# Kernel tuning notes

Hardware: AMD Instinct MI355X
Metric: run time of the kernel (lower is better)

## Reference

```python
import jax, jax.numpy as jnp
import numpy as np

B, S, D = 512, 8, 1024
L = 6        # n_layers
LOOPS = 4    # n_loops
EPS = 1e-5   # LayerNorm eps (torch default)


def setup_inputs() -> dict:
    key = jax.random.key(0)
    ks = jax.random.split(key, 8)
    s = 1.0 / np.sqrt(D)  # torch Linear default init bound
    x = jax.random.normal(ks[0], (B, S, D), jnp.float32)
    gamma = jnp.ones((L, D), jnp.float32)
    beta = jnp.zeros((L, D), jnp.float32)
    Wg = jax.random.uniform(ks[1], (L, D, D), jnp.float32, -s, s)
    bg = jax.random.uniform(ks[2], (L, D), jnp.float32, -s, s)
    Wt = jax.random.uniform(ks[3], (L, D, D), jnp.float32, -s, s)
    bt = jax.random.uniform(ks[4], (L, D), jnp.float32, -s, s)
    Wc = jax.random.uniform(ks[5], (D, 1), jnp.float32, -s, s)
    bc = jax.random.uniform(ks[6], (1,), jnp.float32, -s, s)
    return {"x": x, "gamma": gamma, "beta": beta, "Wg": Wg, "bg": bg,
            "Wt": Wt, "bt": bt, "Wc": Wc, "bc": bc}


def _block(x, gamma, beta, Wg, bg, Wt, bt):
    # LayerNorm over last dim
    mu = jnp.mean(x, axis=-1, keepdims=True)
    var = jnp.mean(jnp.square(x - mu), axis=-1, keepdims=True)
    xn = (x - mu) * jax.lax.rsqrt(var + EPS) * gamma + beta
    g = jax.nn.sigmoid(jnp.einsum('bsd,de->bse', xn, Wg) + bg)
    t = jnp.tanh(jnp.einsum('bsd,de->bse', xn, Wt) + bt)
    return x * (1.0 - g) + t * g


def reference(x, gamma, beta, Wg, bg, Wt, bt, Wc, bc):
    confs = []
    for _ in range(LOOPS):
        for i in range(L):
            x = _block(x, gamma[i], beta[i], Wg[i], bg[i], Wt[i], bt[i])
        # confidence = sigmoid(Linear(x.mean(dim=1)))  -> (B, 1)
        confs.append(jax.nn.sigmoid(x.mean(axis=1) @ Wc + bc))
    return x, jnp.stack(confs)  # ((B,S,D), (LOOPS,B,1))
```

## Files before the change

### kernel.cpp

```cpp
#include <hip/hip_runtime.h>
#include <hip/hip_bf16.h>
#include <math.h>

#define B_ 512
#define S_ 8
#define D_ 1024
#define L_ 6
#define LOOPS_ 4
#define R_ (B_*S_)
#define LD_ (L_*D_)
#define EPSV 1e-5f

#define BM 128
#define BN 128
#define BK 64
#define NT (D_/BK)
#define A_USH 8192
#define B_USH 16384

typedef __attribute__((ext_vector_type(4))) float f32x4;
typedef __attribute__((ext_vector_type(8))) _Float16 f16x8;

__device__ __forceinline__ float bf2f(unsigned short u){
  union { float f; unsigned int i; } v; v.i = ((unsigned int)u) << 16; return v.f;
}
__device__ __forceinline__ unsigned short f2h(float f){
  _Float16 h = (_Float16)f;
  union { _Float16 h; unsigned short u; } v; v.h = h; return v.u;
}
__device__ __forceinline__ float h2f(unsigned short u){
  union { unsigned short u; _Float16 h; } v; v.u = u; return (float)v.h;
}
__device__ __forceinline__ float loadf(const void* p, size_t i, int bf){
  return bf ? bf2f(((const unsigned short*)p)[i]) : ((const float*)p)[i];
}
__device__ __forceinline__ void gload16(const void* g, void* l){
  __builtin_amdgcn_global_load_lds((const __attribute__((address_space(1))) void*)g,
                                   (__attribute__((address_space(3))) void*)l, 16, 0, 0);
}

__global__ void k_detect(const unsigned int* __restrict__ gamma_raw, int* __restrict__ flag){
  if (threadIdx.x == 0 && blockIdx.x == 0)
    *flag = (gamma_raw[0] == 0x3F803F80u) ? 1 : 0;
}

__global__ void k_x2f(const void* __restrict__ x, float* __restrict__ xf,
                      const int* __restrict__ flag, int n4){
  int i = blockIdx.x * blockDim.x + threadIdx.x;
  if (i >= n4) return;
  if (*flag){
    ushort4 u = ((const ushort4*)x)[i];
    float4 f; f.x = bf2f(u.x); f.y = bf2f(u.y); f.z = bf2f(u.z); f.w = bf2f(u.w);
    ((float4*)xf)[i] = f;
  } else {
    ((float4*)xf)[i] = ((const float4*)x)[i];
  }
}

__global__ void k_small(const void* g, const void* b, const void* bgp, const void* btp,
                        const void* wcp, const void* bcp,
                        float* __restrict__ sm, const int* __restrict__ flag){
  int i = blockIdx.x * blockDim.x + threadIdx.x;
  int bf = *flag;
  if (i < LD_)               sm[i] = loadf(g,   i,          bf);
  else if (i < 2*LD_)        sm[i] = loadf(b,   i - LD_,    bf);
  else if (i < 3*LD_)        sm[i] = loadf(bgp, i - 2*LD_,  bf);
  else if (i < 4*LD_)        sm[i] = loadf(btp, i - 3*LD_,  bf);
  else if (i < 4*LD_ + D_)   sm[i] = loadf(wcp, i - 4*LD_,  bf);
  else if (i == 4*LD_ + D_)  sm[i] = loadf(bcp, 0,          bf);
}

__global__ void k_transpose(const void* __restrict__ Wg, const void* __restrict__ Wt,
                            ushort* __restrict__ WgT, ushort* __restrict__ WtT,
                            const float* __restrict__ sm, const int* __restrict__ flag){
  __shared__ ushort tile[32][33];
  int bf = *flag;
  int z = blockIdx.z;
  const void* src; ushort* dst; int lz;
  size_t base;
  if (z < L_) { src = Wg; dst = WgT + (size_t)z * D_ * D_;        base = (size_t)z * D_ * D_; lz = z; }
  else        { src = Wt; dst = WtT + (size_t)(z - L_) * D_ * D_; base = (size_t)(z - L_) * D_ * D_; lz = z - L_; }
  int d0 = blockIdx.y * 32, e0 = blockIdx.x * 32;
  int tx = threadIdx.x, ty = threadIdx.y;
  #pragma unroll
  for (int i = 0; i < 4; i++){
    int r = ty + i * 8;
    size_t idx = base + (size_t)(d0 + r) * D_ + e0 + tx;
    float v = bf ? bf2f(((const ushort*)src)[idx]) : ((const float*)src)[idx];
    float gv = sm[(size_t)lz * D_ + d0 + r];
    tile[r][tx] = f2h(gv * v);
  }
  __syncthreads();
  #pragma unroll
  for (int i = 0; i < 4; i++){
    int r = ty + i * 8;
    dst[(size_t)(e0 + r) * D_ + d0 + tx] = tile[tx][r];
  }
}

__global__ __launch_bounds__(256) void k_bias(const ushort* __restrict__ WgT, const ushort* __restrict__ WtT,
                      const float* __restrict__ sm, float* __restrict__ bias2){
  int idx = blockIdx.x * 256 + threadIdx.x;
  int mat = idx / LD_;
  int rem = idx - mat * LD_;
  int l = rem >> 10, e = rem & 1023;
  const ushort* WT = (mat ? WtT : WgT) + (size_t)l * D_ * D_ + (size_t)e * D_;
  const float* beta = sm + LD_ + (size_t)l * D_;
  float acc = sm[(size_t)(2 + mat) * LD_ + rem];
  for (int d = 0; d < D_; d++)
    acc += beta[d] * h2f(WT[d]);
  bias2[idx] = acc;
}

__device__ __forceinline__ void stage_Bh(const ushort* __restrict__ wsrc,
    ushort* __restrict__ dstbase, int nbase, int kb, int w, int lane)
{
  int rr = lane >> 3;
  int clog = (lane & 7) ^ rr;
  int coff = kb + clog * 8;
  int r0 = w * 16;
  gload16(wsrc + (size_t)(nbase + r0 + rr) * D_ + coff,     dstbase + r0 * 64);
  gload16(wsrc + (size_t)(nbase + r0 + 8 + rr) * D_ + coff, dstbase + (r0 + 8) * 64);
}

__global__ __launch_bounds__(512, 2) void k_gemm_gate(
    const float* __restrict__ xin, float* __restrict__ xout,
    const ushort* __restrict__ WgT, const ushort* __restrict__ WtT,
    const float* __restrict__ bgf, const float* __restrict__ btf)
{
  __shared__ __align__(16) ushort smem[2 * A_USH + 3 * B_USH];

  const int t = threadIdx.x;
  const int lane = t & 63, w = t >> 6;
  const int wrr = (w >> 2) * 64, wnn = (w & 3) * 32;
  const int l15 = lane & 15;

  int bid = blockIdx.x;
  int swz = (bid & 7) * 32 + (bid >> 3);
  int mbase = (swz >> 3) * BM;
  int nbase = (swz & 7) * BN;

  ushort* Abuf = smem;
  ushort* Bbuf = smem + 2 * A_USH;

  float mu = 0.f, rs = 0.f;
  {
    const float* xb = xin + (size_t)(mbase + w * 16) * D_;
    for (int j = 0; j < 16; j++){
      float s = 0.f, q = 0.f;
      #pragma unroll
      for (int p = 0; p < 4; p++){
        float4 v = *(const float4*)(xb + (size_t)j * D_ + p * 256 + lane * 4);
        s += v.x + v.y + v.z + v.w;
        q += v.x * v.x + v.y * v.y + v.z * v.z + v.w * v.w;
      }
      #pragma unroll
      for (int o = 32; o; o >>= 1){ s += __shfl_xor(s, o); q += __shfl_xor(q, o); }
      float m = s * (1.0f / D_);
      float r2 = rsqrtf(q * (1.0f / D_) - m * m + EPSV);
      if ((lane >> 2) == j){ mu = m; rs = r2; }
    }
  }

  const int ar = t >> 2, cq = t & 3;
  const float* xrow = xin + (size_t)(mbase + ar) * D_;

  f32x4 accg[4][2], acct[4][2];
  #pragma unroll
  for (int i = 0; i < 4; i++)
    #pragma unroll
    for (int j = 0; j < 2; j++){
      accg[i][j] = (f32x4){0.f, 0.f, 0.f, 0.f};
      acct[i][j] = (f32x4){0.f, 0.f, 0.f, 0.f};
    }

  float4 ra[4];
  f16x8 af0[4], bg0[2], bt0[2];
  f16x8 af1[4], bg1[2], bt1[2];

  #pragma unroll
  for (int i = 0; i < 2; i++)
    #pragma unroll
    for (int j = 0; j < 2; j++)
      ra[i * 2 + j] = *(const float4*)(xrow + (cq + i * 4) * 8 + j * 4);
  stage_Bh(WgT, Bbuf, nbase, 0, w, lane);
  stage_Bh(WtT, Bbuf + 8192, nbase, 0, w, lane);
  stage_Bh(WgT, Bbuf + B_USH, nbase, BK, w, lane);
  stage_Bh(WtT, Bbuf + B_USH + 8192, nbase, BK, w, lane);
  asm volatile("s_waitcnt vmcnt(8)" ::: "memory");
  #pragma unroll
  for (int i = 0; i < 2; i++){
    int c = cq + i * 4;
    float4 a0 = ra[i * 2], a1 = ra[i * 2 + 1];
    f16x8 hv;
    hv[0] = (_Float16)((a0.x - mu) * rs); hv[1] = (_Float16)((a0.y - mu) * rs);
    hv[2] = (_Float16)((a0.z - mu) * rs); hv[3] = (_Float16)((a0.w - mu) * rs);
    hv[4] = (_Float16)((a1.x - mu) * rs); hv[5] = (_Float16)((a1.y - mu) * rs);
    hv[6] = (_Float16)((a1.z - mu) * rs); hv[7] = (_Float16)((a1.w - mu) * rs);
    *(f16x8*)(Abuf + ar * 64 + ((c ^ (ar & 7)) << 3)) = hv;
  }
  asm volatile("s_waitcnt vmcnt(4)" ::: "memory");
  __builtin_amdgcn_s_barrier();
  {
    int cl = (lane >> 4);
    #pragma unroll
    for (int mf = 0; mf < 4; mf++){
      int r = wrr + mf * 16 + l15;
      af0[mf] = *(const f16x8*)(Abuf + r * 64 + ((cl ^ (r & 7)) << 3));
    }
    #pragma unroll
    for (int nf = 0; nf < 2; nf++){
      int r = wnn + nf * 16 + l15;
      int off = r * 64 + ((cl ^ (r & 7)) << 3);
      bg0[nf] = *(const f16x8*)(Bbuf + off);
      bt0[nf] = *(const f16x8*)(Bbuf + 8192 + off);
    }
  }

  for (int kt = 0; kt < NT; ++kt){
    ushort* Ab = Abuf + (kt & 1) * A_USH;
    ushort* An = Abuf + ((kt + 1) & 1) * A_USH;
    ushort* Bb = Bbuf + (kt % 3) * B_USH;
    ushort* Bn1 = Bbuf + ((kt + 1) % 3) * B_USH;
    ushort* Bn2 = Bbuf + ((kt + 2) % 3) * B_USH;

    {
      int cl = 4 + (lane >> 4);
      #pragma unroll
      for (int mf = 0; mf < 4; mf++){
        int r = wrr + mf * 16 + l15;
        af1[mf] = *(const f16x8*)(Ab + r * 64 + ((cl ^ (r & 7)) << 3));
      }
      #pragma unroll
      for (int nf = 0; nf < 2; nf++){
        int r = wnn + nf * 16 + l15;
        int off = r * 64 + ((cl ^ (r & 7)) << 3);
        bg1[nf] = *(const f16x8*)(Bb + off);
        bt1[nf] = *(const f16x8*)(Bb + 8192 + off);
      }
    }
    if (kt + 1 < NT){
      int kb = (kt + 1) * BK;
      #pragma unroll
      for (int i = 0; i < 2; i++)
        #pragma unroll
        for (int j = 0; j < 2; j++)
          ra[i * 2 + j] = *(const float4*)(xrow + kb + (cq + i * 4) * 8 + j * 4);
    }
    if (kt + 2 < NT) stage_Bh(WgT, Bn2, nbase, (kt + 2) * BK, w, lane);
    __builtin_amdgcn_s_setprio(1);
    #pragma unroll
    for (int mf = 0; mf < 4; mf++)
      #pragma unroll
      for (int nf = 0; nf < 2; nf++){
        accg[mf][nf] = __builtin_amdgcn_mfma_f32_16x16x32_f16(af0[mf], bg0[nf], accg[mf][nf], 0, 0, 0);
        acct[mf][nf] = __builtin_amdgcn_mfma_f32_16x16x32_f16(af0[mf], bt0[nf], acct[mf][nf], 0, 0, 0);
      }
    __builtin_amdgcn_s_setprio(0);

    if (kt + 2 < NT) stage_Bh(WtT, Bn2 + 8192, nbase, (kt + 2) * BK, w, lane);
    if (kt + 1 < NT){
      if (kt == NT - 2) asm volatile("s_waitcnt vmcnt(0)" ::: "memory");
      else              asm volatile("s_waitcnt vmcnt(4)" ::: "memory");
      #pragma unroll
      for (int i = 0; i < 2; i++){
        int c = cq + i * 4;
        float4 a0 = ra[i * 2], a1 = ra[i * 2 + 1];
        f16x8 hv;
        hv[0] = (_Float16)((a0.x - mu) * rs); hv[1] = (_Float16)((a0.y - mu) * rs);
        hv[2] = (_Float16)((a0.z - mu) * rs); hv[3] = (_Float16)((a0.w - mu) * rs);
        hv[4] = (_Float16)((a1.x - mu) * rs); hv[5] = (_Float16)((a1.y - mu) * rs);
        hv[6] = (_Float16)((a1.z - mu) * rs); hv[7] = (_Float16)((a1.w - mu) * rs);
        *(f16x8*)(An + ar * 64 + ((c ^ (ar & 7)) << 3)) = hv;
      }
    }
    __builtin_amdgcn_s_barrier();
    if (kt + 1 < NT){
      int cl = (lane >> 4);
      #pragma unroll
      for (int mf = 0; mf < 4; mf++){
        int r = wrr + mf * 16 + l15;
        af0[mf] = *(const f16x8*)(An + r * 64 + ((cl ^ (r & 7)) << 3));
      }
      #pragma unroll
      for (int nf = 0; nf < 2; nf++){
        int r = wnn + nf * 16 + l15;
        int off = r * 64 + ((cl ^ (r & 7)) << 3);
        bg0[nf] = *(const f16x8*)(Bn1 + off);
        bt0[nf] = *(const f16x8*)(Bn1 + 8192 + off);
      }
    }
    __builtin_amdgcn_s_setprio(1);
    #pragma unroll
    for (int mf = 0; mf < 4; mf++)
      #pragma unroll
      for (int nf = 0; nf < 2; nf++){
        accg[mf][nf] = __builtin_amdgcn_mfma_f32_16x16x32_f16(af1[mf], bg1[nf], accg[mf][nf], 0, 0, 0);
        acct[mf][nf] = __builtin_amdgcn_mfma_f32_16x16x32_f16(af1[mf], bt1[nf], acct[mf][nf], 0, 0, 0);
      }
    __builtin_amdgcn_s_setprio(0);
  }

  #pragma unroll
  for (int mf = 0; mf < 4; mf++){
    int row0 = mbase + wrr + mf * 16 + ((lane >> 4) * 4);
    #pragma unroll
    for (int nf = 0; nf < 2; nf++){
      int col = nbase + wnn + nf * 16 + l15;
      float bgv = bgf[col];
      float btv = btf[col];
      #pragma unroll
      for (int j = 0; j < 4; j++){
        float ug = accg[mf][nf][j] + bgv;
        float ut = acct[mf][nf][j] + btv;
        float g = 1.0f / (1.0f + expf(-ug));
        float tt = tanhf(ut);
        size_t idx = (size_t)(row0 + j) * D_ + col;
        float xo = xin[idx];
        xout[idx] = xo + g * (tt - xo);
      }
    }
  }
}

__global__ __launch_bounds__(256) void k_conf(const float* __restrict__ xf, const float* __restrict__ Wc,
                       const float* __restrict__ bc, float* __restrict__ out, int loop){
  int b = blockIdx.x;
  int t = threadIdx.x;
  const float* xb = xf + (size_t)b * S_ * D_;
  float acc = 0.f;
  for (int i = t; i < S_ * D_; i += 256){
    int d = i & (D_ - 1);
    acc += xb[i] * Wc[d];
  }
  #pragma unroll
  for (int o = 32; o; o >>= 1) acc += __shfl_xor(acc, o);
  __shared__ float wsum[4];
  int w = t >> 6, lane = t & 63;
  if (lane == 0) wsum[w] = acc;
  __syncthreads();
  if (t == 0){
    float s = wsum[0] + wsum[1] + wsum[2] + wsum[3];
    float z = s * (1.0f / S_) + bc[0];
    float c = 1.0f / (1.0f + expf(-z));
    out[(size_t)R_ * D_ + (size_t)loop * B_ + b] = c;
  }
}

__global__ void k_f2x(const float* __restrict__ xf, float* __restrict__ out, int n4){
  int i = blockIdx.x * blockDim.x + threadIdx.x;
  if (i >= n4) return;
  ((float4*)out)[i] = ((const float4*)xf)[i];
}

extern "C" void kernel_launch(void* const* d_in, const int* in_sizes, int n_in,
                              void* d_out, int out_size, void* d_ws, size_t ws_size,
                              hipStream_t stream){
  const void* x     = d_in[0];
  const void* gamma = d_in[1];
  const void* beta  = d_in[2];
  const void* Wg    = d_in[3];
  const void* bg    = d_in[4];
  const void* Wt    = d_in[5];
  const void* bt    = d_in[6];
  const void* Wc    = d_in[7];
  const void* bc    = d_in[8];
  float* out = (float*)d_out;

  char* ws = (char*)d_ws;
  float*  xfA = (float*)ws;
  float*  xfB = xfA + (size_t)R_ * D_;
  ushort* WgT = (ushort*)(xfB + (size_t)R_ * D_);
  ushort* WtT = WgT + (size_t)L_ * D_ * D_;
  float*  sm  = (float*)(WtT + (size_t)L_ * D_ * D_);
  float*  bias2 = sm + 4 * LD_ + D_ + 1;
  int*    flag  = (int*)(bias2 + 2 * LD_);

  k_detect<<<1, 64, 0, stream>>>((const unsigned int*)gamma, flag);
  k_small<<<(4 * LD_ + D_ + 1 + 255) / 256, 256, 0, stream>>>(gamma, beta, bg, bt, Wc, bc, sm, flag);
  k_x2f<<<4096, 256, 0, stream>>>(x, xfA, flag, R_ * D_ / 4);
  dim3 tb(32, 8); dim3 tg(D_ / 32, D_ / 32, 2 * L_);
  k_transpose<<<tg, tb, 0, stream>>>(Wg, Wt, WgT, WtT, sm, flag);
  k_bias<<<2 * LD_ / 256, 256, 0, stream>>>(WgT, WtT, sm, bias2);

  const float* smWc = sm + 4 * LD_;
  const float* smBc = sm + 4 * LD_ + D_;

  for (int loop = 0; loop < LOOPS_; ++loop){
    for (int l = 0; l < L_; ++l){
      int step = loop * L_ + l;
      const float* xin = (step & 1) ? xfB : xfA;
      float*       xo  = (step & 1) ? xfA : xfB;
      k_gemm_gate<<<256, 512, 0, stream>>>(xin, xo,
                                           WgT + (size_t)l * D_ * D_, WtT + (size_t)l * D_ * D_,
                                           bias2 + (size_t)l * D_, bias2 + (size_t)(L_ + l) * D_);
    }
    k_conf<<<B_, 256, 0, stream>>>(xfA, smWc, smBc, out, loop);
  }
  k_f2x<<<4096, 256, 0, stream>>>(xfA, out, R_ * D_ / 4);
}
```

Baseline: 1.060 ms.

## Fuse LayerNorm row statistics into GEMM epilogue and restructure k-loop pipeline

Each gated GEMM now writes per-row partial sums and sums of squares for its output column block. The next layer reads these eight partials instead of re-reading whole rows of x to compute LayerNorm statistics, and the initial conversion kernel produces the first set. The main loop is reorganised to load both k-substeps at once and stage Wg/Wt together, launch bounds change to one block per CU, and sigmoid/tanh use fast __expf forms. The bias precompute is also parallelised across a wavefront. The trade-off is extra shuffle and shared-memory reductions in the epilogue, and a different register and occupancy profile.

```diff
diff --git a/kernel.cpp b/kernel.cpp
--- a/kernel.cpp
+++ b/kernel.cpp
@@ -28,9 +28,6 @@
   _Float16 h = (_Float16)f;
   union { _Float16 h; unsigned short u; } v; v.h = h; return v.u;
 }
-__device__ __forceinline__ float h2f(unsigned short u){
-  union { unsigned short u; _Float16 h; } v; v.u = u; return (float)v.h;
-}
 __device__ __forceinline__ float loadf(const void* p, size_t i, int bf){
   return bf ? bf2f(((const unsigned short*)p)[i]) : ((const float*)p)[i];
 }
@@ -38,23 +35,47 @@
   __builtin_amdgcn_global_load_lds((const __attribute__((address_space(1))) void*)g,
                                    (__attribute__((address_space(3))) void*)l, 16, 0, 0);
 }
+__device__ __forceinline__ float fsigmoid(float u){
+  return 1.0f / (1.0f + __expf(-u));
+}
+__device__ __forceinline__ float ftanh(float u){
+  return 1.0f - 2.0f / (__expf(2.0f * u) + 1.0f);
+}
 
 __global__ void k_detect(const unsigned int* __restrict__ gamma_raw, int* __restrict__ flag){
   if (threadIdx.x == 0 && blockIdx.x == 0)
     *flag = (gamma_raw[0] == 0x3F803F80u) ? 1 : 0;
 }
 
-__global__ void k_x2f(const void* __restrict__ x, float* __restrict__ xf,
-                      const int* __restrict__ flag, int n4){
-  int i = blockIdx.x * blockDim.x + threadIdx.x;
-  if (i >= n4) return;
+__global__ __launch_bounds__(256) void k_x2f(const void* __restrict__ x, float* __restrict__ xf,
+                      const int* __restrict__ flag, float* __restrict__ st0){
+  int row = blockIdx.x, t = threadIdx.x;
+  size_t i4 = (size_t)row * 256 + t;
+  float4 v;
   if (*flag){
-    ushort4 u = ((const ushort4*)x)[i];
-    float4 f; f.x = bf2f(u.x); f.y = bf2f(u.y); f.z = bf2f(u.z); f.w = bf2f(u.w);
-    ((float4*)xf)[i] = f;
+    ushort4 u = ((const ushort4*)x)[i4];
+    v.x = bf2f(u.x); v.y = bf2f(u.y); v.z = bf2f(u.z); v.w = bf2f(u.w);
   } else {
-    ((float4*)xf)[i] = ((const float4*)x)[i];
-  }
+    v = ((const float4*)x)[i4];
+  }
+  ((float4*)xf)[i4] = v;
+  float s = v.x + v.y + v.z + v.w;
+  float q = v.x * v.x + v.y * v.y + v.z * v.z + v.w * v.w;
+  #pragma unroll
+  for (int o = 32; o; o >>= 1){ s += __shfl_xor(s, o); q += __shfl_xor(q, o); }
+  __shared__ float ss[4], qq[4];
+  int w = t >> 6, lane = t & 63;
+  if (lane == 0){ ss[w] = s; qq[w] = q; }
+  __syncthreads();
+  if (t == 0){
+    st0[(size_t)row * 2]     = ss[0] + ss[1] + ss[2] + ss[3];
+    st0[(size_t)row * 2 + 1] = qq[0] + qq[1] + qq[2] + qq[3];
+  }
+}
+
+__global__ void k_zstat(float* __restrict__ statsA){
+  int i = blockIdx.x * 256 + threadIdx.x;
+  statsA[2 * R_ + i] = 0.f;
 }
 
 __global__ void k_small(const void* g, const void* b, const void* bgp, const void* btp,
@@ -100,70 +121,74 @@
 
 __global__ __launch_bounds__(256) void k_bias(const ushort* __restrict__ WgT, const ushort* __restrict__ WtT,
                       const float* __restrict__ sm, float* __restrict__ bias2){
-  int idx = blockIdx.x * 256 + threadIdx.x;
+  int w = threadIdx.x >> 6, lane = threadIdx.x & 63;
+  int idx = blockIdx.x * 4 + w;
   int mat = idx / LD_;
   int rem = idx - mat * LD_;
   int l = rem >> 10, e = rem & 1023;
-  const ushort* WT = (mat ? WtT : WgT) + (size_t)l * D_ * D_ + (size_t)e * D_;
-  const float* beta = sm + LD_ + (size_t)l * D_;
-  float acc = sm[(size_t)(2 + mat) * LD_ + rem];
-  for (int d = 0; d < D_; d++)
-    acc += beta[d] * h2f(WT[d]);
-  bias2[idx] = acc;
-}
-
-__device__ __forceinline__ void stage_Bh(const ushort* __restrict__ wsrc,
-    ushort* __restrict__ dstbase, int nbase, int kb, int w, int lane)
+  const ushort* WT = (mat ? WtT : WgT) + (size_t)l * D_ * D_ + (size_t)e * D_ + lane * 16;
+  const float* beta = sm + LD_ + (size_t)l * D_ + lane * 16;
+  float acc = 0.f;
+  #pragma unroll
+  for (int i = 0; i < 2; i++){
+    f16x8 hv = *(const f16x8*)(WT + i * 8);
+    #pragma unroll
+    for (int j = 0; j < 8; j++) acc += beta[i * 8 + j] * (float)hv[j];
+  }
+  #pragma unroll
+  for (int o = 32; o; o >>= 1) acc += __shfl_xor(acc, o);
+  if (lane == 0) bias2[idx] = sm[(size_t)(2 + mat) * LD_ + rem] + acc;
+}
+
+__device__ __forceinline__ void stage_B(const ushort* __restrict__ wg, const ushort* __restrict__ wt,
+    ushort* __restrict__ bbase, int nbase, int kb, int w, int lane)
 {
-  int rr = lane >> 3;
-  int clog = (lane & 7) ^ rr;
-  int coff = kb + clog * 8;
+  int rr = lane >> 3, sl = lane & 7;
+  int coff = kb + ((sl ^ rr) << 3);
   int r0 = w * 16;
-  gload16(wsrc + (size_t)(nbase + r0 + rr) * D_ + coff,     dstbase + r0 * 64);
-  gload16(wsrc + (size_t)(nbase + r0 + 8 + rr) * D_ + coff, dstbase + (r0 + 8) * 64);
-}
-
-__global__ __launch_bounds__(512, 2) void k_gemm_gate(
+  gload16(wg + (size_t)(nbase + r0 + rr) * D_ + coff,     bbase + r0 * 64);
+  gload16(wg + (size_t)(nbase + r0 + 8 + rr) * D_ + coff, bbase + (r0 + 8) * 64);
+  gload16(wt + (size_t)(nbase + r0 + rr) * D_ + coff,     bbase + 8192 + r0 * 64);
+  gload16(wt + (size_t)(nbase + r0 + 8 + rr) * D_ + coff, bbase + 8192 + (r0 + 8) * 64);
+}
+
+__global__ __launch_bounds__(512, 1) void k_gemm_gate(
     const float* __restrict__ xin, float* __restrict__ xout,
     const ushort* __restrict__ WgT, const ushort* __restrict__ WtT,
-    const float* __restrict__ bgf, const float* __restrict__ btf)
+    const float* __restrict__ bgf, const float* __restrict__ btf,
+    const float* __restrict__ stin, float* __restrict__ stout)
 {
   __shared__ __align__(16) ushort smem[2 * A_USH + 3 * B_USH];
+  __shared__ __align__(8) float2 sred[4][128];
 
   const int t = threadIdx.x;
   const int lane = t & 63, w = t >> 6;
-  const int wrr = (w >> 2) * 64, wnn = (w & 3) * 32;
-  const int l15 = lane & 15;
+  const int wr = w >> 2, wn = w & 3;
+  const int l15 = lane & 15, q4 = lane >> 4;
 
   int bid = blockIdx.x;
   int swz = (bid & 7) * 32 + (bid >> 3);
   int mbase = (swz >> 3) * BM;
   int nbase = (swz & 7) * BN;
-
-  ushort* Abuf = smem;
+  int nb = swz & 7;
+
   ushort* Bbuf = smem + 2 * A_USH;
 
-  float mu = 0.f, rs = 0.f;
-  {
-    const float* xb = xin + (size_t)(mbase + w * 16) * D_;
-    for (int j = 0; j < 16; j++){
-      float s = 0.f, q = 0.f;
-      #pragma unroll
-      for (int p = 0; p < 4; p++){
-        float4 v = *(const float4*)(xb + (size_t)j * D_ + p * 256 + lane * 4);
-        s += v.x + v.y + v.z + v.w;
-        q += v.x * v.x + v.y * v.y + v.z * v.z + v.w * v.w;
-      }
-      #pragma unroll
-      for (int o = 32; o; o >>= 1){ s += __shfl_xor(s, o); q += __shfl_xor(q, o); }
-      float m = s * (1.0f / D_);
-      float r2 = rsqrtf(q * (1.0f / D_) - m * m + EPSV);
-      if ((lane >> 2) == j){ mu = m; rs = r2; }
-    }
-  }
-
-  const int ar = t >> 2, cq = t & 3;
-  const float* xrow = xin + (size_t)(mbase + ar) * D_;
+  const int rr8 = lane >> 3, sl = lane & 7;
+  const int ar1 = w * 16 + rr8, ar2 = ar1 + 8;
+  const int clog = sl ^ rr8;
+  float s1 = 0.f, q1 = 0.f, s2 = 0.f, q2 = 0.f;
+  #pragma unroll
+  for (int nb2 = 0; nb2 < 8; nb2++){
+    float2 v1 = *(const float2*)(stin + ((size_t)nb2 * R_ + mbase + ar1) * 2);
+    float2 v2 = *(const float2*)(stin + ((size_t)nb2 * R_ + mbase + ar2) * 2);
+    s1 += v1.x; q1 += v1.y; s2 += v2.x; q2 += v2.y;
+  }
+  float mu1 = s1 * (1.0f / D_), rs1 = rsqrtf(q1 * (1.0f / D_) - mu1 * mu1 + EPSV);
+  float mu2 = s2 * (1.0f / D_), rs2 = rsqrtf(q2 * (1.0f / D_) - mu2 * mu2 + EPSV);
+
+  const float* xr1 = xin + (size_t)(mbase + ar1) * D_ + clog * 8;
+  const float* xr2 = xin + (size_t)(mbase + ar2) * D_ + clog * 8;
 
   f32x4 accg[4][2], acct[4][2];
   #pragma unroll
@@ -174,152 +199,135 @@
       acct[i][j] = (f32x4){0.f, 0.f, 0.f, 0.f};
     }
 
-  float4 ra[4];
-  f16x8 af0[4], bg0[2], bt0[2];
-  f16x8 af1[4], bg1[2], bt1[2];
-
-  #pragma unroll
-  for (int i = 0; i < 2; i++)
-    #pragma unroll
-    for (int j = 0; j < 2; j++)
-      ra[i * 2 + j] = *(const float4*)(xrow + (cq + i * 4) * 8 + j * 4);
-  stage_Bh(WgT, Bbuf, nbase, 0, w, lane);
-  stage_Bh(WtT, Bbuf + 8192, nbase, 0, w, lane);
-  stage_Bh(WgT, Bbuf + B_USH, nbase, BK, w, lane);
-  stage_Bh(WtT, Bbuf + B_USH + 8192, nbase, BK, w, lane);
+  float4 ra0, ra1, ra2, ra3;
+
+  ra0 = *(const float4*)(xr1);     ra1 = *(const float4*)(xr1 + 4);
+  ra2 = *(const float4*)(xr2);     ra3 = *(const float4*)(xr2 + 4);
+  stage_B(WgT, WtT, Bbuf, nbase, 0, w, lane);
+  stage_B(WgT, WtT, Bbuf + B_USH, nbase, BK, w, lane);
   asm volatile("s_waitcnt vmcnt(8)" ::: "memory");
-  #pragma unroll
-  for (int i = 0; i < 2; i++){
-    int c = cq + i * 4;
-    float4 a0 = ra[i * 2], a1 = ra[i * 2 + 1];
-    f16x8 hv;
-    hv[0] = (_Float16)((a0.x - mu) * rs); hv[1] = (_Float16)((a0.y - mu) * rs);
-    hv[2] = (_Float16)((a0.z - mu) * rs); hv[3] = (_Float16)((a0.w - mu) * rs);
-    hv[4] = (_Float16)((a1.x - mu) * rs); hv[5] = (_Float16)((a1.y - mu) * rs);
-    hv[6] = (_Float16)((a1.z - mu) * rs); hv[7] = (_Float16)((a1.w - mu) * rs);
-    *(f16x8*)(Abuf + ar * 64 + ((c ^ (ar & 7)) << 3)) = hv;
+  {
+    f16x8 h1, h2;
+    h1[0]=(_Float16)((ra0.x-mu1)*rs1); h1[1]=(_Float16)((ra0.y-mu1)*rs1);
+    h1[2]=(_Float16)((ra0.z-mu1)*rs1); h1[3]=(_Float16)((ra0.w-mu1)*rs1);
+    h1[4]=(_Float16)((ra1.x-mu1)*rs1); h1[5]=(_Float16)((ra1.y-mu1)*rs1);
+    h1[6]=(_Float16)((ra1.z-mu1)*rs1); h1[7]=(_Float16)((ra1.w-mu1)*rs1);
+    h2[0]=(_Float16)((ra2.x-mu2)*rs2); h2[1]=(_Float16)((ra2.y-mu2)*rs2);
+    h2[2]=(_Float16)((ra2.z-mu2)*rs2); h2[3]=(_Float16)((ra2.w-mu2)*rs2);
+    h2[4]=(_Float16)((ra3.x-mu2)*rs2); h2[5]=(_Float16)((ra3.y-mu2)*rs2);
+    h2[6]=(_Float16)((ra3.z-mu2)*rs2); h2[7]=(_Float16)((ra3.w-mu2)*rs2);
+    *(f16x8*)(smem + ar1 * 64 + (sl << 3)) = h1;
+    *(f16x8*)(smem + ar2 * 64 + (sl << 3)) = h2;
   }
   asm volatile("s_waitcnt vmcnt(4)" ::: "memory");
   __builtin_amdgcn_s_barrier();
-  {
-    int cl = (lane >> 4);
-    #pragma unroll
-    for (int mf = 0; mf < 4; mf++){
-      int r = wrr + mf * 16 + l15;
-      af0[mf] = *(const f16x8*)(Abuf + r * 64 + ((cl ^ (r & 7)) << 3));
-    }
-    #pragma unroll
-    for (int nf = 0; nf < 2; nf++){
-      int r = wnn + nf * 16 + l15;
-      int off = r * 64 + ((cl ^ (r & 7)) << 3);
-      bg0[nf] = *(const f16x8*)(Bbuf + off);
-      bt0[nf] = *(const f16x8*)(Bbuf + 8192 + off);
-    }
-  }
 
   for (int kt = 0; kt < NT; ++kt){
-    ushort* Ab = Abuf + (kt & 1) * A_USH;
-    ushort* An = Abuf + ((kt + 1) & 1) * A_USH;
-    ushort* Bb = Bbuf + (kt % 3) * B_USH;
-    ushort* Bn1 = Bbuf + ((kt + 1) % 3) * B_USH;
+    ushort* Ab  = smem + (kt & 1) * A_USH;
+    ushort* An  = smem + ((kt + 1) & 1) * A_USH;
+    ushort* Bb  = Bbuf + (kt % 3) * B_USH;
     ushort* Bn2 = Bbuf + ((kt + 2) % 3) * B_USH;
 
-    {
-      int cl = 4 + (lane >> 4);
+    if (kt + 1 < NT){
+      int kb = (kt + 1) * BK;
+      ra0 = *(const float4*)(xr1 + kb);     ra1 = *(const float4*)(xr1 + kb + 4);
+      ra2 = *(const float4*)(xr2 + kb);     ra3 = *(const float4*)(xr2 + kb + 4);
+    }
+    if (kt + 2 < NT) stage_B(WgT, WtT, Bn2, nbase, (kt + 2) * BK, w, lane);
+
+    f16x8 af[2][4], bgr[2][2], btr[2][2];
+    #pragma unroll
+    for (int ks = 0; ks < 2; ks++){
+      int cl = ks * 4 + q4;
       #pragma unroll
       for (int mf = 0; mf < 4; mf++){
-        int r = wrr + mf * 16 + l15;
-        af1[mf] = *(const f16x8*)(Ab + r * 64 + ((cl ^ (r & 7)) << 3));
+        int r = wr * 64 + mf * 16 + l15;
+        af[ks][mf] = *(const f16x8*)(Ab + r * 64 + ((cl ^ (r & 7)) << 3));
       }
       #pragma unroll
       for (int nf = 0; nf < 2; nf++){
-        int r = wnn + nf * 16 + l15;
+        int r = wn * 32 + nf * 16 + l15;
         int off = r * 64 + ((cl ^ (r & 7)) << 3);
-        bg1[nf] = *(const f16x8*)(Bb + off);
-        bt1[nf] = *(const f16x8*)(Bb + 8192 + off);
+        bgr[ks][nf] = *(const f16x8*)(Bb + off);
+        btr[ks][nf] = *(const f16x8*)(Bb + 8192 + off);
       }
     }
+
+    __builtin_amdgcn_s_setprio(1);
+    #pragma unroll
+    for (int ks = 0; ks < 2; ks++)
+      #pragma unroll
+      for (int mf = 0; mf < 4; mf++)
+        #pragma unroll
+        for (int nf = 0; nf < 2; nf++){
+          accg[mf][nf] = __builtin_amdgcn_mfma_f32_16x16x32_f16(af[ks][mf], bgr[ks][nf], accg[mf][nf], 0, 0, 0);
+          acct[mf][nf] = __builtin_amdgcn_mfma_f32_16x16x32_f16(af[ks][mf], btr[ks][nf], acct[mf][nf], 0, 0, 0);
+        }
+    __builtin_amdgcn_s_setprio(0);
+
     if (kt + 1 < NT){
-      int kb = (kt + 1) * BK;
-      #pragma unroll
-      for (int i = 0; i < 2; i++)
-        #pragma unroll
-        for (int j = 0; j < 2; j++)
-          ra[i * 2 + j] = *(const float4*)(xrow + kb + (cq + i * 4) * 8 + j * 4);
-    }
-    if (kt + 2 < NT) stage_Bh(WgT, Bn2, nbase, (kt + 2) * BK, w, lane);
-    __builtin_amdgcn_s_setprio(1);
-    #pragma unroll
-    for (int mf = 0; mf < 4; mf++)
-      #pragma unroll
-      for (int nf = 0; nf < 2; nf++){
-        accg[mf][nf] = __builtin_amdgcn_mfma_f32_16x16x32_f16(af0[mf], bg0[nf], accg[mf][nf], 0, 0, 0);
-        acct[mf][nf] = __builtin_amdgcn_mfma_f32_16x16x32_f16(af0[mf], bt0[nf], acct[mf][nf], 0, 0, 0);
-      }
-    __builtin_amdgcn_s_setprio(0);
-
-    if (kt + 2 < NT) stage_Bh(WtT, Bn2 + 8192, nbase, (kt + 2) * BK, w, lane);
-    if (kt + 1 < NT){
-      if (kt == NT - 2) asm volatile("s_waitcnt vmcnt(0)" ::: "memory");
-      else              asm volatile("s_waitcnt vmcnt(4)" ::: "memory");
-      #pragma unroll
-      for (int i = 0; i < 2; i++){
-        int c = cq + i * 4;
-        float4 a0 = ra[i * 2], a1 = ra[i * 2 + 1];
-        f16x8 hv;
-        hv[0] = (_Float16)((a0.x - mu) * rs); hv[1] = (_Float16)((a0.y - mu) * rs);
-        hv[2] = (_Float16)((a0.z - mu) * rs); hv[3] = (_Float16)((a0.w - mu) * rs);
-        hv[4] = (_Float16)((a1.x - mu) * rs); hv[5] = (_Float16)((a1.y - mu) * rs);
-        hv[6] = (_Float16)((a1.z - mu) * rs); hv[7] = (_Float16)((a1.w - mu) * rs);
-        *(f16x8*)(An + ar * 64 + ((c ^ (ar & 7)) << 3)) = hv;
-      }
+      if (kt + 2 < NT) asm volatile("s_waitcnt vmcnt(4)" ::: "memory");
+      else             asm volatile("s_waitcnt vmcnt(0)" ::: "memory");
+      f16x8 h1, h2;
+      h1[0]=(_Float16)((ra0.x-mu1)*rs1); h1[1]=(_Float16)((ra0.y-mu1)*rs1);
+      h1[2]=(_Float16)((ra0.z-mu1)*rs1); h1[3]=(_Float16)((ra0.w-mu1)*rs1);
+      h1[4]=(_Float16)((ra1.x-mu1)*rs1); h1[5]=(_Float16)((ra1.y-mu1)*rs1);
+      h1[6]=(_Float16)((ra1.z-mu1)*rs1); h1[7]=(_Float16)((ra1.w-mu1)*rs1);
+      h2[0]=(_Float16)((ra2.x-mu2)*rs2); h2[1]=(_Float16)((ra2.y-mu2)*rs2);
+      h2[2]=(_Float16)((ra2.z-mu2)*rs2); h2[3]=(_Float16)((ra2.w-mu2)*rs2);
+      h2[4]=(_Float16)((ra3.x-mu2)*rs2); h2[5]=(_Float16)((ra3.y-mu2)*rs2);
+      h2[6]=(_Float16)((ra3.z-mu2)*rs2); h2[7]=(_Float16)((ra3.w-mu2)*rs2);
+      *(f16x8*)(An + ar1 * 64 + (sl << 3)) = h1;
+      *(f16x8*)(An + ar2 * 64 + (sl << 3)) = h2;
     }
     __builtin_amdgcn_s_barrier();
-    if (kt + 1 < NT){
-      int cl = (lane >> 4);
-      #pragma unroll
-      for (int mf = 0; mf < 4; mf++){
-        int r = wrr + mf * 16 + l15;
-        af0[mf] = *(const f16x8*)(An + r * 64 + ((cl ^ (r & 7)) << 3));
-      }
-      #pragma unroll
-      for (int nf = 0; nf < 2; nf++){
-        int r = wnn + nf * 16 + l15;
-        int off = r * 64 + ((cl ^ (r & 7)) << 3);
-        bg0[nf] = *(const f16x8*)(Bn1 + off);
-        bt0[nf] = *(const f16x8*)(Bn1 + 8192 + off);
-      }
-    }
-    __builtin_amdgcn_s_setprio(1);
-    #pragma unroll
-    for (int mf = 0; mf < 4; mf++)
-      #pragma unroll
-      for (int nf = 0; nf < 2; nf++){
-        accg[mf][nf] = __builtin_amdgcn_mfma_f32_16x16x32_f16(af1[mf], bg1[nf], accg[mf][nf], 0, 0, 0);
-        acct[mf][nf] = __builtin_amdgcn_mfma_f32_16x16x32_f16(af1[mf], bt1[nf], acct[mf][nf], 0, 0, 0);
-      }
-    __builtin_amdgcn_s_setprio(0);
-  }
+  }
+
+  float ps[16], pq[16];
+  #pragma unroll
+  for (int i = 0; i < 16; i++){ ps[i] = 0.f; pq[i] = 0.f; }
 
   #pragma unroll
   for (int mf = 0; mf < 4; mf++){
-    int row0 = mbase + wrr + mf * 16 + ((lane >> 4) * 4);
+    int row0 = mbase + wr * 64 + mf * 16 + q4 * 4;
     #pragma unroll
     for (int nf = 0; nf < 2; nf++){
-      int col = nbase + wnn + nf * 16 + l15;
+      int col = nbase + wn * 32 + nf * 16 + l15;
       float bgv = bgf[col];
       float btv = btf[col];
       #pragma unroll
       for (int j = 0; j < 4; j++){
-        float ug = accg[mf][nf][j] + bgv;
-        float ut = acct[mf][nf][j] + btv;
-        float g = 1.0f / (1.0f + expf(-ug));
-        float tt = tanhf(ut);
+        float g  = fsigmoid(accg[mf][nf][j] + bgv);
+        float tt = ftanh(acct[mf][nf][j] + btv);
         size_t idx = (size_t)(row0 + j) * D_ + col;
         float xo = xin[idx];
-        xout[idx] = xo + g * (tt - xo);
+        float v = xo + g * (tt - xo);
+        xout[idx] = v;
+        ps[mf * 4 + j] += v;
+        pq[mf * 4 + j] += v * v;
       }
     }
+  }
+  #pragma unroll
+  for (int i = 0; i < 16; i++){
+    #pragma unroll
+    for (int o = 1; o < 16; o <<= 1){
+      ps[i] += __shfl_xor(ps[i], o);
+      pq[i] += __shfl_xor(pq[i], o);
+    }
+  }
+  if (l15 == 0){
+    #pragma unroll
+    for (int mf = 0; mf < 4; mf++)
+      #pragma unroll
+      for (int j = 0; j < 4; j++)
+        sred[wn][wr * 64 + mf * 16 + q4 * 4 + j] = make_float2(ps[mf * 4 + j], pq[mf * 4 + j]);
+  }
+  __syncthreads();
+  if (t < 128){
+    float2 a = sred[0][t], b2 = sred[1][t], c = sred[2][t], d = sred[3][t];
+    float2 r = make_float2(a.x + b2.x + c.x + d.x, a.y + b2.y + c.y + d.y);
+    *(float2*)(stout + ((size_t)nb * R_ + mbase + t) * 2) = r;
   }
 }
 
@@ -342,8 +350,7 @@
   if (t == 0){
     float s = wsum[0] + wsum[1] + wsum[2] + wsum[3];
     float z = s * (1.0f / S_) + bc[0];
-    float c = 1.0f / (1.0f + expf(-z));
-    out[(size_t)R_ * D_ + (size_t)loop * B_ + b] = c;
+    out[(size_t)R_ * D_ + (size_t)loop * B_ + b] = fsigmoid(z);
   }
 }
 
@@ -372,16 +379,19 @@
   float*  xfB = xfA + (size_t)R_ * D_;
   ushort* WgT = (ushort*)(xfB + (size_t)R_ * D_);
   ushort* WtT = WgT + (size_t)L_ * D_ * D_;
-  float*  sm  = (float*)(WtT + (size_t)L_ * D_ * D_);
+  float*  statsA = (float*)(WtT + (size_t)L_ * D_ * D_);
+  float*  statsB = statsA + 8 * R_ * 2;
+  float*  sm  = statsB + 8 * R_ * 2;
   float*  bias2 = sm + 4 * LD_ + D_ + 1;
   int*    flag  = (int*)(bias2 + 2 * LD_);
 
   k_detect<<<1, 64, 0, stream>>>((const unsigned int*)gamma, flag);
   k_small<<<(4 * LD_ + D_ + 1 + 255) / 256, 256, 0, stream>>>(gamma, beta, bg, bt, Wc, bc, sm, flag);
-  k_x2f<<<4096, 256, 0, stream>>>(x, xfA, flag, R_ * D_ / 4);
+  k_x2f<<<R_, 256, 0, stream>>>(x, xfA, flag, statsA);
+  k_zstat<<<7 * R_ * 2 / 256, 256, 0, stream>>>(statsA);
   dim3 tb(32, 8); dim3 tg(D_ / 32, D_ / 32, 2 * L_);
   k_transpose<<<tg, tb, 0, stream>>>(Wg, Wt, WgT, WtT, sm, flag);
-  k_bias<<<2 * LD_ / 256, 256, 0, stream>>>(WgT, WtT, sm, bias2);
+  k_bias<<<2 * LD_ / 4, 256, 0, stream>>>(WgT, WtT, sm, bias2);
 
   const float* smWc = sm + 4 * LD_;
   const float* smBc = sm + 4 * LD_ + D_;
@@ -391,9 +401,12 @@
       int step = loop * L_ + l;
       const float* xin = (step & 1) ? xfB : xfA;
       float*       xo  = (step & 1) ? xfA : xfB;
+      const float* sin = (step & 1) ? statsB : statsA;
+      float*       so  = (step & 1) ? statsA : statsB;
       k_gemm_gate<<<256, 512, 0, stream>>>(xin, xo,
                                            WgT + (size_t)l * D_ * D_, WtT + (size_t)l * D_ * D_,
-                                           bias2 + (size_t)l * D_, bias2 + (size_t)(L_ + l) * D_);
+                                           bias2 + (size_t)l * D_, bias2 + (size_t)(L_ + l) * D_,
+                                           sin, so);
     }
     k_conf<<<B_, 256, 0, stream>>>(xfA, smWc, smBc, out, loop);
   }
```

Measured after the change: 907.5 us. -14.4%, faster.
